# Optimization experiments

Measured on AMD Instinct MI355X. Metric: run time of the kernel, lower is better.

The kernel has to match this reference:

```python
import jax, jax.numpy as jnp
import numpy as np

EPS = 1e-12  # matches torch.nn.functional.normalize default eps


def _l2norm(x, axis=-1):
    # F.normalize: x / max(||x||, eps)
    n = jnp.sqrt(jnp.sum(x * x, axis=axis, keepdims=True))
    return x / jnp.maximum(n, EPS)


def setup_inputs() -> dict:
    key = jax.random.key(0)
    k1, k2, k3 = jax.random.split(key, 3)
    batch, n_mels, time_steps = 32, 80, 4000
    num_codebooks, codebook_size, d = 2, 1024, 64
    mel = jax.random.normal(k1, (batch, n_mels, time_steps), dtype=jnp.float32)
    proj = jax.random.normal(k2, (num_codebooks, n_mels, d), dtype=jnp.float32)
    codebooks = jax.random.normal(k3, (num_codebooks, codebook_size, d), dtype=jnp.float32)
    return {"mel": mel, "proj": proj, "codebooks": codebooks}


def reference(mel, proj, codebooks):
    # mel: [b, n, t] -> [b, t, n]
    mel_t = jnp.transpose(mel, (0, 2, 1))
    # project for all codebooks at once: [c, b, t, d]
    p = jnp.einsum('btn,cnd->cbtd', mel_t, proj)
    p = _l2norm(p, axis=-1)
    cb = _l2norm(codebooks, axis=-1)  # [c, k, d]
    # cosine similarity: [c, b, t, k]
    sim = jnp.einsum('cbtd,ckd->cbtk', p, cb)
    codes = jnp.argmax(sim, axis=-1)  # [c, b, t]
    return codes
```

## Files before the change

kernel.cpp:

```cpp
#include <hip/hip_runtime.h>
#include <hip/hip_bf16.h>
#include <math.h>
#include <stdint.h>


#define B      32
#define NMELS  80
#define TSTEPS 4000
#define NCB    2
#define KCB    1024
#define DDIM   64
#define TPB    256
#define TM     64
#define KT     64
#define NKT    (KCB / KT)
#define PPAD   66

typedef short bf16x8 __attribute__((ext_vector_type(8)));
typedef float f32x4  __attribute__((ext_vector_type(4)));

#define WS_CB_OFF   8192
#define WS_NEEDED   (8192 + NCB*KCB*DDIM*2)

static __device__ __forceinline__ uint32_t bits(float f) {
    return __builtin_bit_cast(uint32_t, f);
}
static __device__ __forceinline__ float fbits(uint32_t u) {
    return __builtin_bit_cast(float, u);
}
static __device__ __forceinline__ uint32_t rne16(uint32_t u) {
    return (u + 0x7FFFu + ((u >> 16) & 1u)) >> 16;
}

__global__ __launch_bounds__(TPB) void rpq_prep(const float* __restrict__ cb,
                                                float* __restrict__ ws)
{
    const int idx = blockIdx.x * TPB + threadIdx.x;
    if (idx >= NCB * KCB) return;

    const float4* row = (const float4*)(cb + (size_t)idx * DDIM);
    float4 v[16];
    float ss = 0.f;
    #pragma unroll
    for (int i = 0; i < 16; ++i) {
        v[i] = row[i];
        ss += v[i].x*v[i].x + v[i].y*v[i].y + v[i].z*v[i].z + v[i].w*v[i].w;
    }
    const float inv = 1.0f / fmaxf(sqrtf(ss), 1e-12f);
    ws[idx] = inv;

    uint32_t dw[32];
    #pragma unroll
    for (int i = 0; i < 16; ++i) {
        dw[2*i]   = rne16(bits(v[i].x * inv)) | (rne16(bits(v[i].y * inv)) << 16);
        dw[2*i+1] = rne16(bits(v[i].z * inv)) | (rne16(bits(v[i].w * inv)) << 16);
    }
    uint4* dst = (uint4*)((char*)ws + WS_CB_OFF + (size_t)idx * 128);
    #pragma unroll
    for (int i = 0; i < 8; ++i)
        dst[i] = make_uint4(dw[4*i], dw[4*i+1], dw[4*i+2], dw[4*i+3]);
}

__global__ __launch_bounds__(TPB, 3) void rpq_main(
    const float* __restrict__ mel,
    const float* __restrict__ proj,
    const float* __restrict__ cb,
    const float* __restrict__ ws,
    int* __restrict__ out)
{
    const int tid  = threadIdx.x;
    const int b    = blockIdx.y;
    const int c    = blockIdx.z;
    const int t0   = blockIdx.x * TM;

    const int l    = tid & 63;
    const int wid  = tid >> 6;
    const int lrow = l & 15;
    const int lgrp = l >> 4;

    __shared__ union __align__(16) {
        float projS[NMELS * DDIM];
        struct {
            char  cbuf[2][KT * 128];
            float PL[TM * PPAD];
        } p2;
    } U;
    __shared__ float    invnS[KCB];
    __shared__ uint32_t cand[TM][17][2];
    __shared__ float    scv[TM][8];
    __shared__ int      sck[TM][8];

    const char* wscb = (const char*)ws + WS_CB_OFF + (size_t)c * (KCB * 128);

    {
        const float4* src = (const float4*)(proj + (size_t)c * NMELS * DDIM);
        float4* dst = (float4*)U.projS;
        for (int i = tid; i < NMELS * DDIM / 4; i += TPB) dst[i] = src[i];
        *(float4*)&invnS[4 * tid] = *(const float4*)(ws + (size_t)c * KCB + 4 * tid);
    }
    __syncthreads();

    const int srow = tid >> 2;
    const int sq   = tid & 3;
    uint4 g0, g1;
    {
        const uint4* gp = (const uint4*)(wscb + (size_t)srow * 128 + sq * 32);
        g0 = gp[0]; g1 = gp[1];
    }

    {
        const int tl = tid & 63, dq = tid >> 6;
        const int tg = t0 + tl;
        const int tc = (tg < TSTEPS) ? tg : (TSTEPS - 1);
        float Pa[16];
        #pragma unroll
        for (int i = 0; i < 16; ++i) Pa[i] = 0.f;
        const float* mp = mel + (size_t)b * NMELS * TSTEPS + tc;
        for (int n = 0; n < NMELS; ++n) {
            const float m = mp[(size_t)n * TSTEPS];
            const float* ps = &U.projS[n * DDIM + dq * 16];
            #pragma unroll
            for (int i = 0; i < 16; ++i) Pa[i] = fmaf(m, ps[i], Pa[i]);
        }
        __syncthreads();
        #pragma unroll
        for (int i = 0; i < 16; i += 4)
            *(float4*)&U.p2.PL[tl * PPAD + dq * 16 + i] =
                make_float4(Pa[i], Pa[i+1], Pa[i+2], Pa[i+3]);
    }

    {
        const int xw = (srow & 7) << 4;
        char* base = &U.p2.cbuf[0][srow * 128];
        *(uint4*)(base + ((sq * 32)      ^ xw)) = g0;
        *(uint4*)(base + ((sq * 32 + 16) ^ xw)) = g1;
    }
    __syncthreads();

    bf16x8 A0, A1;
    {
        const float* pr = &U.p2.PL[((wid << 4) + lrow) * PPAD];
        #pragma unroll
        for (int i = 0; i < 8; ++i) {
            A0[i] = (short)rne16(bits(pr[lgrp * 8 + i]));
            A1[i] = (short)rne16(bits(pr[32 + lgrp * 8 + i]));
        }
    }

    float m1[4], m2[4];
    #pragma unroll
    for (int r = 0; r < 4; ++r) { m1[r] = -INFINITY; m2[r] = -INFINITY; }
    uint32_t idxv = (uint32_t)(1023 - lrow);

    const int xr  = (lrow & 7) << 4;
    const int bo0 = (lgrp * 16) ^ xr;
    const int bo1 = (64 + lgrp * 16) ^ xr;

    for (int kt = 0; kt < NKT; ++kt) {
        const int cur = kt & 1;
        if (kt + 1 < NKT) {
            const uint4* gp = (const uint4*)(wscb + (size_t)(kt + 1) * (KT * 128)
                                             + (size_t)srow * 128 + sq * 32);
            g0 = gp[0]; g1 = gp[1];
        }
        const char* buf = U.p2.cbuf[cur];
        #pragma unroll
        for (int s = 0; s < 4; ++s) {
            const char* rowp = buf + (s * 16 + lrow) * 128;
            bf16x8 B0 = *(const bf16x8*)(rowp + bo0);
            bf16x8 B1 = *(const bf16x8*)(rowp + bo1);
            f32x4 acc = {0.f, 0.f, 0.f, 0.f};
            acc = __builtin_amdgcn_mfma_f32_16x16x32_bf16(A0, B0, acc, 0, 0, 0);
            acc = __builtin_amdgcn_mfma_f32_16x16x32_bf16(A1, B1, acc, 0, 0, 0);
            #pragma unroll
            for (int r = 0; r < 4; ++r) {
                const float pf = fbits((bits(acc[r]) & 0xFFFFFC00u) | idxv);
                m2[r] = __builtin_amdgcn_fmed3f(pf, m1[r], m2[r]);
                m1[r] = fmaxf(pf, m1[r]);
            }
            idxv -= 16u;
        }
        if (kt + 1 < NKT) {
            const int xw = (srow & 7) << 4;
            char* base = &U.p2.cbuf[cur ^ 1][srow * 128];
            *(uint4*)(base + ((sq * 32)      ^ xw)) = g0;
            *(uint4*)(base + ((sq * 32 + 16) ^ xw)) = g1;
        }
        __syncthreads();
    }

    #pragma unroll
    for (int r = 0; r < 4; ++r) {
        const int trow = (wid << 4) + (lgrp << 2) + r;
        cand[trow][lrow][0] = bits(m1[r]);
        cand[trow][lrow][1] = bits(m2[r]);
    }
    __syncthreads();

    {
        const int t = tid & 63;
        const int j = wid;
        float c1 = -INFINITY, c2 = -INFINITY, c3 = -INFINITY, c4 = -INFINITY;
        float c5 = -INFINITY, c6 = -INFINITY, c7 = -INFINITY, c8 = -INFINITY;
        for (int i = 0; i < 16; ++i) {
            #pragma unroll
            for (int jj = 0; jj < 2; ++jj) {
                const float p = fbits(cand[t][i][jj]);
                c8 = fmaxf(fminf(p, c7), c8);
                c7 = fmaxf(fminf(p, c6), c7);
                c6 = fmaxf(fminf(p, c5), c6);
                c5 = fmaxf(fminf(p, c4), c5);
                c4 = fmaxf(fminf(p, c3), c4);
                c3 = fmaxf(fminf(p, c2), c3);
                c2 = fmaxf(fminf(p, c1), c2);
                c1 = fmaxf(p, c1);
            }
        }
        const float sel0 = (j == 0) ? c1 : (j == 1) ? c3 : (j == 2) ? c5 : c7;
        const float sel1 = (j == 0) ? c2 : (j == 1) ? c4 : (j == 2) ? c6 : c8;
        const float* pr = &U.p2.PL[t * PPAD];
        const float* cbc = cb + (size_t)c * KCB * DDIM;
        #pragma unroll
        for (int e = 0; e < 2; ++e) {
            const float sel = e ? sel1 : sel0;
            const int kj = 1023 - (int)(bits(sel) & 0x3FFu);
            const float* cbr = cbc + (size_t)kj * DDIM;
            float a0 = 0.f, a1 = 0.f, a2 = 0.f, a3 = 0.f;
            #pragma unroll
            for (int i = 0; i < 16; ++i) {
                float4 pv = *(const float4*)(pr + i * 4);
                float4 cv = *(const float4*)(cbr + i * 4);
                a0 = fmaf(pv.x, cv.x, a0); a1 = fmaf(pv.y, cv.y, a1);
                a2 = fmaf(pv.z, cv.z, a2); a3 = fmaf(pv.w, cv.w, a3);
            }
            scv[t][2*j + e] = ((a0 + a1) + (a2 + a3)) * invnS[kj];
            sck[t][2*j + e] = kj;
        }
    }
    __syncthreads();

    if (tid < TM) {
        const int tg = t0 + tid;
        if (tg < TSTEPS) {
            float best = scv[tid][0];
            int   bk   = sck[tid][0];
            #pragma unroll
            for (int s2 = 1; s2 < 8; ++s2) {
                const float v = scv[tid][s2];
                const int  kk = sck[tid][s2];
                if (v > best || (v == best && kk < bk)) { best = v; bk = kk; }
            }
            out[((size_t)c * B + b) * TSTEPS + tg] = bk;
        }
    }
}

__global__ __launch_bounds__(TPB, 2) void rpq_fallback(
    const float* __restrict__ mel, const float* __restrict__ proj,
    const float* __restrict__ cb, int* __restrict__ out)
{
    const int tid = threadIdx.x;
    const int b = blockIdx.y, c = blockIdx.z;
    const int t0 = blockIdx.x * (TPB * 2) + tid;
    const int t1 = t0 + TPB;
    const int tc0 = (t0 < TSTEPS) ? t0 : (TSTEPS - 1);
    const int tc1 = (t1 < TSTEPS) ? t1 : (TSTEPS - 1);

    __shared__ union { float projS[NMELS*DDIM]; float cbS[2][64*DDIM]; } sh;
    __shared__ float invn[KCB];
    const float* cbc = cb + (size_t)c * KCB * DDIM;
    {
        const float4* src = (const float4*)(proj + (size_t)c * NMELS * DDIM);
        float4* dst = (float4*)sh.projS;
        for (int i = tid; i < NMELS*DDIM/4; i += TPB) dst[i] = src[i];
    }
    for (int j = 0; j < KCB/TPB; ++j) {
        const int k = j*TPB + tid;
        const float4* r = (const float4*)(cbc + (size_t)k * DDIM);
        float s = 0.f;
        #pragma unroll
        for (int i = 0; i < DDIM/4; ++i) {
            float4 v = r[i]; s += v.x*v.x + v.y*v.y + v.z*v.z + v.w*v.w;
        }
        invn[k] = 1.0f / fmaxf(sqrtf(s), 1e-12f);
    }
    float4 r0, r1, r2, r3;
    { const float4* g = (const float4*)cbc;
      r0 = g[tid]; r1 = g[tid+256]; r2 = g[tid+512]; r3 = g[tid+768]; }
    __syncthreads();
    float P0[DDIM], P1[DDIM];
    #pragma unroll
    for (int d = 0; d < DDIM; ++d) { P0[d] = 0.f; P1[d] = 0.f; }
    const float* mp = mel + (size_t)b * NMELS * TSTEPS;
    for (int n = 0; n < NMELS; ++n) {
        const float m0 = mp[(size_t)n*TSTEPS + tc0];
        const float m1_ = mp[(size_t)n*TSTEPS + tc1];
        const float4* ps = (const float4*)(sh.projS + n*DDIM);
        #pragma unroll
        for (int i = 0; i < DDIM/4; ++i) {
            float4 v = ps[i];
            P0[4*i+0]=fmaf(m0,v.x,P0[4*i+0]); P0[4*i+1]=fmaf(m0,v.y,P0[4*i+1]);
            P0[4*i+2]=fmaf(m0,v.z,P0[4*i+2]); P0[4*i+3]=fmaf(m0,v.w,P0[4*i+3]);
            P1[4*i+0]=fmaf(m1_,v.x,P1[4*i+0]); P1[4*i+1]=fmaf(m1_,v.y,P1[4*i+1]);
            P1[4*i+2]=fmaf(m1_,v.z,P1[4*i+2]); P1[4*i+3]=fmaf(m1_,v.w,P1[4*i+3]);
        }
    }
    __syncthreads();
    { float4* dst = (float4*)sh.cbS[0];
      dst[tid]=r0; dst[tid+256]=r1; dst[tid+512]=r2; dst[tid+768]=r3; }
    { const float4* g = (const float4*)(cbc + (size_t)64*DDIM);
      r0=g[tid]; r1=g[tid+256]; r2=g[tid+512]; r3=g[tid+768]; }
    __syncthreads();
    float best0 = -INFINITY, best1 = -INFINITY; int bi0 = 0, bi1 = 0;
    for (int kt = 0; kt < KCB/64; ++kt) {
        const int cur = kt & 1;
        const float* base = sh.cbS[cur];
        const int kbase = kt * 64;
        #pragma unroll 2
        for (int kk = 0; kk < 64; ++kk) {
            const float4* row = (const float4*)(base + kk*DDIM);
            float a0=0,a1=0,a2=0,a3=0,b0=0,b1=0,b2=0,b3=0;
            #pragma unroll
            for (int i = 0; i < DDIM/4; ++i) {
                float4 v = row[i];
                a0=fmaf(P0[4*i+0],v.x,a0); a1=fmaf(P0[4*i+1],v.y,a1);
                a2=fmaf(P0[4*i+2],v.z,a2); a3=fmaf(P0[4*i+3],v.w,a3);
                b0=fmaf(P1[4*i+0],v.x,b0); b1=fmaf(P1[4*i+1],v.y,b1);
                b2=fmaf(P1[4*i+2],v.z,b2); b3=fmaf(P1[4*i+3],v.w,b3);
            }
            const int k = kbase + kk;
            const float w = invn[k];
            const float s0 = ((a0+a1)+(a2+a3))*w;
            const float s1 = ((b0+b1)+(b2+b3))*w;
            if (s0 > best0) { best0 = s0; bi0 = k; }
            if (s1 > best1) { best1 = s1; bi1 = k; }
        }
        if (kt + 1 < KCB/64) {
            float4* dst = (float4*)sh.cbS[cur ^ 1];
            dst[tid]=r0; dst[tid+256]=r1; dst[tid+512]=r2; dst[tid+768]=r3;
            if (kt + 2 < KCB/64) {
                const float4* g = (const float4*)(cbc + (size_t)(kt+2)*64*DDIM);
                r0=g[tid]; r1=g[tid+256]; r2=g[tid+512]; r3=g[tid+768];
            }
        }
        __syncthreads();
    }
    const size_t ob = ((size_t)c * B + b) * TSTEPS;
    if (t0 < TSTEPS) out[ob + t0] = bi0;
    if (t1 < TSTEPS) out[ob + t1] = bi1;
}

extern "C" void kernel_launch(void* const* d_in, const int* in_sizes, int n_in,
                              void* d_out, int out_size, void* d_ws, size_t ws_size,
                              hipStream_t stream) {
    const float* mel  = (const float*)d_in[0];
    const float* proj = (const float*)d_in[1];
    const float* cb   = (const float*)d_in[2];
    int* out = (int*)d_out;

    if (ws_size >= (size_t)WS_NEEDED) {
        float* ws = (float*)d_ws;
        rpq_prep<<<dim3((NCB*KCB + TPB - 1)/TPB), dim3(TPB), 0, stream>>>(cb, ws);
        dim3 grid((TSTEPS + TM - 1) / TM, B, NCB);
        rpq_main<<<grid, dim3(TPB), 0, stream>>>(mel, proj, cb, ws, out);
    } else {
        dim3 grid((TSTEPS + TPB*2 - 1) / (TPB*2), B, NCB);
        rpq_fallback<<<grid, dim3(TPB), 0, stream>>>(mel, proj, cb, out);
    }
}
```

Baseline: 175.5 us.

## Alias post-loop LDS buffers, drop invnS, retile projection for occupancy 4

Places the candidate and score scratch arrays in a union with the codebook double buffer, and reads the inverse codebook norms from global memory instead of staging them in LDS. This shrinks shared memory per block so launch bounds can be raised from 3 to 4 blocks per CU. The projection stage is also retiled so each thread computes a 4x4 tile (4 timesteps by 4 dims) with float4 mel loads, in place of 16 dims for 1 timestep. The cost is an extra uncoalesced global load per candidate and tighter register limits, which could cause spills.

```diff
diff --git a/kernel.cpp b/kernel.cpp
--- a/kernel.cpp
+++ b/kernel.cpp
@@ -61,7 +61,7 @@
         dst[i] = make_uint4(dw[4*i], dw[4*i+1], dw[4*i+2], dw[4*i+3]);
 }
 
-__global__ __launch_bounds__(TPB, 3) void rpq_main(
+__global__ __launch_bounds__(TPB, 4) void rpq_main(
     const float* __restrict__ mel,
     const float* __restrict__ proj,
     const float* __restrict__ cb,
@@ -81,22 +81,25 @@
     __shared__ union __align__(16) {
         float projS[NMELS * DDIM];
         struct {
-            char  cbuf[2][KT * 128];
+            union {
+                char cbuf[2][KT * 128];
+                struct {
+                    uint32_t cand[TM][17][2];
+                    float    scv[TM][8];
+                    int      sck[TM][8];
+                } m;
+            } a;
             float PL[TM * PPAD];
         } p2;
     } U;
-    __shared__ float    invnS[KCB];
-    __shared__ uint32_t cand[TM][17][2];
-    __shared__ float    scv[TM][8];
-    __shared__ int      sck[TM][8];
-
-    const char* wscb = (const char*)ws + WS_CB_OFF + (size_t)c * (KCB * 128);
+
+    const char*  wscb   = (const char*)ws + WS_CB_OFF + (size_t)c * (KCB * 128);
+    const float* invn_g = ws + (size_t)c * KCB;
 
     {
         const float4* src = (const float4*)(proj + (size_t)c * NMELS * DDIM);
         float4* dst = (float4*)U.projS;
         for (int i = tid; i < NMELS * DDIM / 4; i += TPB) dst[i] = src[i];
-        *(float4*)&invnS[4 * tid] = *(const float4*)(ws + (size_t)c * KCB + 4 * tid);
     }
     __syncthreads();
 
@@ -109,29 +112,41 @@
     }
 
     {
-        const int tl = tid & 63, dq = tid >> 6;
-        const int tg = t0 + tl;
-        const int tc = (tg < TSTEPS) ? tg : (TSTEPS - 1);
-        float Pa[16];
-        #pragma unroll
-        for (int i = 0; i < 16; ++i) Pa[i] = 0.f;
-        const float* mp = mel + (size_t)b * NMELS * TSTEPS + tc;
+        const int tq = tid & 15;
+        const int dg = tid >> 4;
+        const int tbase  = t0 + tq * 4;
+        const int tb_c   = (tbase <= TSTEPS - 4) ? tbase : (TSTEPS - 4);
+        const float* mp  = mel + (size_t)b * NMELS * TSTEPS + tb_c;
+
+        float Pa[4][4];
+        #pragma unroll
+        for (int i = 0; i < 4; ++i)
+            #pragma unroll
+            for (int j = 0; j < 4; ++j) Pa[i][j] = 0.f;
+
         for (int n = 0; n < NMELS; ++n) {
-            const float m = mp[(size_t)n * TSTEPS];
-            const float* ps = &U.projS[n * DDIM + dq * 16];
-            #pragma unroll
-            for (int i = 0; i < 16; ++i) Pa[i] = fmaf(m, ps[i], Pa[i]);
+            const float4 m4 = *(const float4*)(mp + (size_t)n * TSTEPS);
+            const float4 w  = *(const float4*)&U.projS[n * DDIM + dg * 4];
+            Pa[0][0] = fmaf(m4.x, w.x, Pa[0][0]); Pa[0][1] = fmaf(m4.x, w.y, Pa[0][1]);
+            Pa[0][2] = fmaf(m4.x, w.z, Pa[0][2]); Pa[0][3] = fmaf(m4.x, w.w, Pa[0][3]);
+            Pa[1][0] = fmaf(m4.y, w.x, Pa[1][0]); Pa[1][1] = fmaf(m4.y, w.y, Pa[1][1]);
+            Pa[1][2] = fmaf(m4.y, w.z, Pa[1][2]); Pa[1][3] = fmaf(m4.y, w.w, Pa[1][3]);
+            Pa[2][0] = fmaf(m4.z, w.x, Pa[2][0]); Pa[2][1] = fmaf(m4.z, w.y, Pa[2][1]);
+            Pa[2][2] = fmaf(m4.z, w.z, Pa[2][2]); Pa[2][3] = fmaf(m4.z, w.w, Pa[2][3]);
+            Pa[3][0] = fmaf(m4.w, w.x, Pa[3][0]); Pa[3][1] = fmaf(m4.w, w.y, Pa[3][1]);
+            Pa[3][2] = fmaf(m4.w, w.z, Pa[3][2]); Pa[3][3] = fmaf(m4.w, w.w, Pa[3][3]);
         }
         __syncthreads();
-        #pragma unroll
-        for (int i = 0; i < 16; i += 4)
-            *(float4*)&U.p2.PL[tl * PPAD + dq * 16 + i] =
-                make_float4(Pa[i], Pa[i+1], Pa[i+2], Pa[i+3]);
+
+        #pragma unroll
+        for (int i = 0; i < 4; ++i)
+            *(float4*)&U.p2.PL[(tq * 4 + i) * PPAD + dg * 4] =
+                make_float4(Pa[i][0], Pa[i][1], Pa[i][2], Pa[i][3]);
     }
 
     {
         const int xw = (srow & 7) << 4;
-        char* base = &U.p2.cbuf[0][srow * 128];
+        char* base = &U.p2.a.cbuf[0][srow * 128];
         *(uint4*)(base + ((sq * 32)      ^ xw)) = g0;
         *(uint4*)(base + ((sq * 32 + 16) ^ xw)) = g1;
     }
@@ -163,7 +178,7 @@
                                              + (size_t)srow * 128 + sq * 32);
             g0 = gp[0]; g1 = gp[1];
         }
-        const char* buf = U.p2.cbuf[cur];
+        const char* buf = U.p2.a.cbuf[cur];
         #pragma unroll
         for (int s = 0; s < 4; ++s) {
             const char* rowp = buf + (s * 16 + lrow) * 128;
@@ -182,7 +197,7 @@
         }
         if (kt + 1 < NKT) {
             const int xw = (srow & 7) << 4;
-            char* base = &U.p2.cbuf[cur ^ 1][srow * 128];
+            char* base = &U.p2.a.cbuf[cur ^ 1][srow * 128];
             *(uint4*)(base + ((sq * 32)      ^ xw)) = g0;
             *(uint4*)(base + ((sq * 32 + 16) ^ xw)) = g1;
         }
@@ -192,8 +207,8 @@
     #pragma unroll
     for (int r = 0; r < 4; ++r) {
         const int trow = (wid << 4) + (lgrp << 2) + r;
-        cand[trow][lrow][0] = bits(m1[r]);
-        cand[trow][lrow][1] = bits(m2[r]);
+        U.p2.a.m.cand[trow][lrow][0] = bits(m1[r]);
+        U.p2.a.m.cand[trow][lrow][1] = bits(m2[r]);
     }
     __syncthreads();
 
@@ -205,7 +220,7 @@
         for (int i = 0; i < 16; ++i) {
             #pragma unroll
             for (int jj = 0; jj < 2; ++jj) {
-                const float p = fbits(cand[t][i][jj]);
+                const float p = fbits(U.p2.a.m.cand[t][i][jj]);
                 c8 = fmaxf(fminf(p, c7), c8);
                 c7 = fmaxf(fminf(p, c6), c7);
                 c6 = fmaxf(fminf(p, c5), c6);
@@ -218,7 +233,7 @@
         }
         const float sel0 = (j == 0) ? c1 : (j == 1) ? c3 : (j == 2) ? c5 : c7;
         const float sel1 = (j == 0) ? c2 : (j == 1) ? c4 : (j == 2) ? c6 : c8;
-        const float* pr = &U.p2.PL[t * PPAD];
+        const float* pr  = &U.p2.PL[t * PPAD];
         const float* cbc = cb + (size_t)c * KCB * DDIM;
         #pragma unroll
         for (int e = 0; e < 2; ++e) {
@@ -233,8 +248,8 @@
                 a0 = fmaf(pv.x, cv.x, a0); a1 = fmaf(pv.y, cv.y, a1);
                 a2 = fmaf(pv.z, cv.z, a2); a3 = fmaf(pv.w, cv.w, a3);
             }
-            scv[t][2*j + e] = ((a0 + a1) + (a2 + a3)) * invnS[kj];
-            sck[t][2*j + e] = kj;
+            U.p2.a.m.scv[t][2*j + e] = ((a0 + a1) + (a2 + a3)) * invn_g[kj];
+            U.p2.a.m.sck[t][2*j + e] = kj;
         }
     }
     __syncthreads();
@@ -242,12 +257,12 @@
     if (tid < TM) {
         const int tg = t0 + tid;
         if (tg < TSTEPS) {
-            float best = scv[tid][0];
-            int   bk   = sck[tid][0];
+            float best = U.p2.a.m.scv[tid][0];
+            int   bk   = U.p2.a.m.sck[tid][0];
             #pragma unroll
             for (int s2 = 1; s2 < 8; ++s2) {
-                const float v = scv[tid][s2];
-                const int  kk = sck[tid][s2];
+                const float v = U.p2.a.m.scv[tid][s2];
+                const int  kk = U.p2.a.m.sck[tid][s2];
                 if (v > best || (v == best && kk < bk)) { best = v; bk = kk; }
             }
             out[((size_t)c * B + b) * TSTEPS + tg] = bk;
```

After: 167.7 us. 4.5% less time.
